# Kernel optimization log

Hardware: AMD Instinct MI355X
Metric: run time of the kernel (lower is better)

## Reference

```python
import jax, jax.numpy as jnp
import numpy as np

N = 50000          # nodes
E = 800000         # edges (avg degree 16)
NFEAT = 128        # dim_touched / gcn_nfeat
NHID = 96
NCLASS = 64
EXTRA = 32         # extra MLP-only features
NHID1, NHID2 = 128, 64
NN = 70            # top-k threshold rank
EPS = 1e-5         # BatchNorm1d eps


def setup_inputs() -> dict:
    key = jax.random.key(0)
    ks = jax.random.split(key, 24)
    x = jax.random.normal(ks[0], (N, NFEAT + EXTRA + 1), jnp.float32)
    grp = jax.random.randint(ks[1], (N,), 0, 2).astype(jnp.float32)
    x = x.at[:, -1].set(grp)  # last column is the group flag (target_group == 0)
    row = jax.random.randint(ks[2], (E,), 0, N, dtype=jnp.int32)
    col = jax.random.randint(ks[3], (E,), 0, N, dtype=jnp.int32)
    val = jax.random.uniform(ks[4], (E,), jnp.float32)

    def p(k, shape):
        return (jax.random.normal(k, shape, jnp.float32) * 0.05)

    return dict(
        x=x, row=row, col=col, val=val,
        W1=p(ks[5], (NFEAT, NHID)), b1=p(ks[6], (NHID,)),
        W2=p(ks[7], (NHID, NHID)), b2=p(ks[8], (NHID,)),
        W3=p(ks[9], (NHID, NHID)), b3=p(ks[10], (NHID,)),
        W4=p(ks[11], (NHID, NHID)), b4=p(ks[12], (NHID,)),
        W5=p(ks[13], (NHID, NCLASS)), b5=p(ks[14], (NCLASS,)),
        M1w=p(ks[15], (NCLASS + EXTRA, NHID1)), M1b=p(ks[16], (NHID1,)),
        M2w=p(ks[17], (NHID1, NHID2)), M2b=p(ks[18], (NHID2,)),
        M3w=p(ks[19], (NHID2, 1)), M3b=p(ks[20], (1,)),
    )


def _bn(h):
    # fresh BatchNorm1d in training mode, affine at default init (gamma=1, beta=0)
    m = jnp.mean(h, axis=0)
    v = jnp.mean((h - m) ** 2, axis=0)  # biased variance, as used for normalization
    return (h - m) * jax.lax.rsqrt(v + EPS)


def _gc(h, row, col, val, W, b):
    # GraphConvolution: spmm(adj, h @ W) + b, adj in COO form
    s = h @ W                                            # [N, out]
    msg = val[:, None] * s[col]                          # [E, out]
    agg = jax.ops.segment_sum(msg, row, num_segments=N)  # [N, out]
    return agg + b


def reference(x, row, col, val, W1, b1, W2, b2, W3, b3, W4, b4, W5, b5,
              M1w, M1b, M2w, M2b, M3w, M3b):
    h = x[:, :NFEAT]
    h = _bn(jax.nn.relu(_gc(h, row, col, val, W1, b1)))
    h = _bn(jax.nn.relu(_gc(h, row, col, val, W2, b2)))
    h = _bn(jax.nn.relu(_gc(h, row, col, val, W3, b3)))
    h = _bn(jax.nn.relu(_gc(h, row, col, val, W4, b4)))
    h = jax.nn.relu(_gc(h, row, col, val, W5, b5))        # [N, NCLASS]

    feat = jnp.concatenate([h, x[:, NFEAT:-1]], axis=1)   # [N, NCLASS+EXTRA]
    m = jax.nn.relu(feat @ M1w + M1b)
    m = jax.nn.relu(m @ M2w + M2b)
    m = m @ M3w + M3b                                     # [N, 1]

    # mask out target_group rows with the global min
    m = jnp.where(x[:, -1:] == 0.0, jnp.min(m), m)        # [N, 1]

    # top-70 threshold: value at descending rank NN
    thresh = jax.lax.top_k(m[:, 0], NN + 1)[0][NN]
    recip = jax.lax.stop_gradient(1.0 / m)                # torch reciprocal on detach()
    mask = jnp.where(m > thresh, recip, jnp.zeros_like(m))
    return m * mask
```

## Files before the change

kernel.cpp:

```cpp
#include <hip/hip_runtime.h>
#include <cstdint>
#include <cstddef>

#define XLD 161
#define GA  3072

typedef float f4u __attribute__((ext_vector_type(4), aligned(4)));
typedef float f4a __attribute__((ext_vector_type(4)));
typedef float f3u __attribute__((ext_vector_type(3), aligned(4)));
typedef float f2a __attribute__((ext_vector_type(2)));

__global__ void hist_kernel(const int* __restrict__ row, int* __restrict__ cnt, int E) {
    for (int e = blockIdx.x * blockDim.x + threadIdx.x; e < E; e += gridDim.x * blockDim.x)
        atomicAdd(&cnt[row[e]], 1);
}

__global__ __launch_bounds__(256)
void scan1_kernel(const int* __restrict__ cnt, int* __restrict__ offs,
                  int* __restrict__ bsums, int n) {
    int t = threadIdx.x;
    int gid = blockIdx.x * 256 + t;
    int v = (gid < n) ? cnt[gid] : 0;
    int x = v;
#pragma unroll
    for (int o = 1; o < 64; o <<= 1) { int y = __shfl_up(x, o); if ((t & 63) >= o) x += y; }
    __shared__ int ws[4];
    if ((t & 63) == 63) ws[t >> 6] = x;
    __syncthreads();
    int add = 0;
    for (int w = 0; w < (t >> 6); w++) add += ws[w];
    int incl = x + add;
    if (gid < n) offs[gid] = incl - v;
    if (t == 255) bsums[blockIdx.x] = incl;
}

__global__ __launch_bounds__(256)
void scan2_kernel(int* __restrict__ bsums, int nb) {
    int t = threadIdx.x;
    int v = (t < nb) ? bsums[t] : 0;
    int x = v;
#pragma unroll
    for (int o = 1; o < 64; o <<= 1) { int y = __shfl_up(x, o); if ((t & 63) >= o) x += y; }
    __shared__ int ws[4];
    if ((t & 63) == 63) ws[t >> 6] = x;
    __syncthreads();
    int add = 0;
    for (int w = 0; w < (t >> 6); w++) add += ws[w];
    if (t < nb) bsums[t] = x + add - v;
}

__global__ void scan3_kernel(int* __restrict__ offs, int* __restrict__ cursor,
                             const int* __restrict__ bsums, int n, int E) {
    int gid = blockIdx.x * 256 + threadIdx.x;
    if (gid < n) {
        int o = offs[gid] + bsums[blockIdx.x];
        offs[gid] = o;
        cursor[gid] = o;
    }
    if (gid == 0) offs[n] = E;
}

__global__ void scatter_kernel(const int* __restrict__ row, const int* __restrict__ col,
                               const float* __restrict__ val, int* __restrict__ cursor,
                               int2* __restrict__ cvA, int E) {
    for (int e = blockIdx.x * blockDim.x + threadIdx.x; e < E; e += gridDim.x * blockDim.x) {
        int r = row[e];
        int p = atomicAdd(&cursor[r], 1);
        cvA[p] = make_int2(col[e], __float_as_int(val[e]));
    }
}

template <int LC, bool WVS>
__global__ __launch_bounds__(256)
void aggP(const float* __restrict__ S, int ldS, const int* __restrict__ offs,
          const int2* __restrict__ cvA,
          float* __restrict__ Aout, float* __restrict__ vout, int n) {
    int lane = threadIdx.x & 63;
    int lg   = lane & 31;
    int grp  = threadIdx.x >> 5;
    int sh   = lane & 32;

    for (int node = blockIdx.x * 8 + grp; node < n; node += gridDim.x * 8) {
        int e0 = offs[node], e1 = offs[node + 1];
        float acc[LC];
#pragma unroll
        for (int a = 0; a < LC; a++) acc[a] = 0.f;
        float vsum = 0.f;

        for (int e = e0; e < e1; e += 32) {
            int   idx = e + lg;
            int2  cv = (idx < e1) ? cvA[idx] : make_int2(0, 0);
            int   ce = cv.x;
            float ve = __int_as_float(cv.y);
            int   cnt = min(32, e1 - e);
#pragma unroll 8
            for (int j = 0; j < cnt; j++) {
                int   c = __shfl(ce, sh + j);
                float v = __shfl(ve, sh + j);
                const float* srow = S + (size_t)c * ldS + LC * lg;
                if (LC == 3) {
                    f3u g = *(const f3u*)srow;
                    acc[0] = fmaf(v, g[0], acc[0]);
                    acc[1] = fmaf(v, g[1], acc[1]);
                    acc[2] = fmaf(v, g[2], acc[2]);
                } else {
                    f4u g = *(const f4u*)srow;
                    acc[0] = fmaf(v, g[0], acc[0]);
                    acc[1] = fmaf(v, g[1], acc[1]);
                    acc[2] = fmaf(v, g[2], acc[2]);
                    acc[3] = fmaf(v, g[3], acc[3]);
                }
                vsum += v;
            }
        }

        float* orow = Aout + (size_t)node * (32 * LC) + LC * lg;
        if (LC == 3) {
            f3u o; o[0] = acc[0]; o[1] = acc[1]; o[2] = acc[2];
            *(f3u*)orow = o;
        } else {
            f4u o; o[0] = acc[0]; o[1] = acc[1]; o[2] = acc[2]; o[3] = acc[3];
            *(f4u*)orow = o;
        }
        if (WVS && lg == 0) vout[node] = vsum;
    }
}

__global__ __launch_bounds__(256)
void aggB(const float* __restrict__ S, const int* __restrict__ offs,
          const int2* __restrict__ cvA, const float* __restrict__ bias,
          float* __restrict__ Hout, float* __restrict__ vout,
          float* __restrict__ pbuf, int n) {
    __shared__ float sS[96], sQ[96];
    int t = threadIdx.x;
    if (t < 96) { sS[t] = 0.f; sQ[t] = 0.f; }
    __syncthreads();
    int lane = t & 63, lg = lane & 31, grp = t >> 5, sh = lane & 32;
    float bb[3];
    bb[0] = bias[3 * lg]; bb[1] = bias[3 * lg + 1]; bb[2] = bias[3 * lg + 2];
    float ps[3] = {0.f, 0.f, 0.f}, pq[3] = {0.f, 0.f, 0.f};

    for (int node = blockIdx.x * 8 + grp; node < n; node += gridDim.x * 8) {
        int e0 = offs[node], e1 = offs[node + 1];
        float acc[3] = {0.f, 0.f, 0.f};
        float vsum = 0.f;
        for (int e = e0; e < e1; e += 32) {
            int   idx = e + lg;
            int2  cv = (idx < e1) ? cvA[idx] : make_int2(0, 0);
            int   ce = cv.x;
            float ve = __int_as_float(cv.y);
            int   cnt = min(32, e1 - e);
#pragma unroll 8
            for (int j = 0; j < cnt; j++) {
                int   c = __shfl(ce, sh + j);
                float v = __shfl(ve, sh + j);
                const float* srow = S + (size_t)c * 96 + 3 * lg;
                f3u g = *(const f3u*)srow;
                acc[0] = fmaf(v, g[0], acc[0]);
                acc[1] = fmaf(v, g[1], acc[1]);
                acc[2] = fmaf(v, g[2], acc[2]);
                vsum += v;
            }
        }
        float* orow = Hout + (size_t)node * 96 + 3 * lg;
        f3u o;
#pragma unroll
        for (int a = 0; a < 3; a++) {
            float v = fmaxf(acc[a] + bb[a], 0.f);
            o[a] = v;
            ps[a] += v; pq[a] += v * v;
        }
        *(f3u*)orow = o;
        if (lg == 0) vout[node] = vsum;
    }
#pragma unroll
    for (int a = 0; a < 3; a++) {
        atomicAdd(&sS[3 * lg + a], ps[a]);
        atomicAdd(&sQ[3 * lg + a], pq[a]);
    }
    __syncthreads();
    if (t < 96) {
        pbuf[(size_t)t * GA + blockIdx.x]        = sS[t];
        pbuf[(size_t)(96 + t) * GA + blockIdx.x] = sQ[t];
    }
}

__global__ __launch_bounds__(256)
void bn_reduce(const float* __restrict__ pbuf, float* __restrict__ bsum,
               float* __restrict__ bsumsq) {
    int j = blockIdx.x;
    const float* rowp = pbuf + (size_t)j * GA;
    float s = 0.f;
    for (int i = threadIdx.x; i < GA; i += 256) s += rowp[i];
#pragma unroll
    for (int o = 32; o; o >>= 1) s += __shfl_down(s, o);
    __shared__ float ws[4];
    if ((threadIdx.x & 63) == 0) ws[threadIdx.x >> 6] = s;
    __syncthreads();
    if (threadIdx.x == 0) {
        float tot = ws[0] + ws[1] + ws[2] + ws[3];
        if (j < 96) bsum[j] = tot; else bsumsq[j - 96] = tot;
    }
}

__global__ __launch_bounds__(256)
void aggC(const float* __restrict__ S, const int* __restrict__ offs,
          const int2* __restrict__ cvA, const float* __restrict__ bias,
          const float* __restrict__ cb, const float* __restrict__ vsum,
          float* __restrict__ Hout, int n) {
    int lane = threadIdx.x & 63, lg = lane & 31, grp = threadIdx.x >> 5, sh = lane & 32;
    float bb0 = bias[2 * lg], bb1 = bias[2 * lg + 1];
    float cc0 = cb[2 * lg],   cc1 = cb[2 * lg + 1];

    for (int node = blockIdx.x * 8 + grp; node < n; node += gridDim.x * 8) {
        int e0 = offs[node], e1 = offs[node + 1];
        float a0 = 0.f, a1 = 0.f;
        for (int e = e0; e < e1; e += 32) {
            int   idx = e + lg;
            int2  cv = (idx < e1) ? cvA[idx] : make_int2(0, 0);
            int   ce = cv.x;
            float ve = __int_as_float(cv.y);
            int   cnt = min(32, e1 - e);
#pragma unroll 8
            for (int j = 0; j < cnt; j++) {
                int   c = __shfl(ce, sh + j);
                float v = __shfl(ve, sh + j);
                f2a g = *(const f2a*)(S + (size_t)c * 64 + 2 * lg);
                a0 = fmaf(v, g[0], a0);
                a1 = fmaf(v, g[1], a1);
            }
        }
        float vs = vsum[node];
        f2a o;
        o[0] = fmaxf(a0 + vs * cc0 + bb0, 0.f);
        o[1] = fmaxf(a1 + vs * cc1 + bb1, 0.f);
        *(f2a*)(Hout + (size_t)node * 64 + 2 * lg) = o;
    }
}

template <int CT>
__device__ inline void ldw(const float* p, float* wv) {
    if constexpr (CT == 4) { *(f4a*)wv = *(const f4a*)p; }
    else if constexpr (CT == 6) { *(f3u*)wv = *(const f3u*)p; *(f3u*)(wv + 3) = *(const f3u*)(p + 3); }
    else { *(f4a*)wv = *(const f4a*)p; *(f4a*)(wv + 4) = *(const f4a*)(p + 4); }
}

template <int K, int C, bool DOBN, bool HASCB, bool LIN = false, bool DOT = false>
__global__ __launch_bounds__(256)
void gemmF(const float* __restrict__ A1, int ld1, int split,
           const float* __restrict__ A2, int ld2,
           const float* __restrict__ W, const float* __restrict__ bias,
           const float* __restrict__ cbv, const float* __restrict__ vsum,
           float* __restrict__ Out, float* __restrict__ bsum,
           float* __restrict__ bsumsq, int n) {
    constexpr int CT = C / 16;
    __shared__ float Wc[16 * C];
    __shared__ float At[16][68];
    __shared__ float redS[DOBN ? C : 1];
    __shared__ float redQ[DOBN ? C : 1];

    int t  = threadIdx.x;
    int tc = t & 15, tr = t >> 4;
    int row0 = blockIdx.x * 64;

    if (DOBN && t < C) { redS[t] = 0.f; redQ[t] = 0.f; }

    int srow = t >> 2;
    int gr = row0 + srow; if (gr >= n) gr = n - 1;
    int kh = (t & 3) * 4;

    float acc[4][CT];
#pragma unroll
    for (int i = 0; i < 4; i++)
#pragma unroll
        for (int c = 0; c < CT; c++) acc[i][c] = 0.f;

    for (int kb = 0; kb < K; kb += 16) {
        __syncthreads();
        for (int i = t * 4; i < 16 * C; i += 1024)
            *(f4a*)&Wc[i] = *(const f4u*)&W[(size_t)kb * C + i];
        {
            int kg = kb + kh;
            const float* src = (kg < split) ? (A1 + (size_t)gr * ld1 + kg)
                                            : (A2 + (size_t)gr * ld2 + (kg - split));
            f4u v = *(const f4u*)src;
#pragma unroll
            for (int e = 0; e < 4; e++) At[kh + e][srow] = v[e];
        }
        __syncthreads();
#pragma unroll
        for (int kk = 0; kk < 16; kk++) {
            f4a av = *(const f4a*)&At[kk][tr * 4];
            float wv[CT];
            ldw<CT>(&Wc[kk * C + tc * CT], wv);
#pragma unroll
            for (int i = 0; i < 4; i++)
#pragma unroll
                for (int c = 0; c < CT; c++) acc[i][c] = fmaf(av[i], wv[c], acc[i][c]);
        }
    }

    if constexpr (DOT) {
        float bb2[CT], ww[CT];
#pragma unroll
        for (int c = 0; c < CT; c++) { bb2[c] = bias[tc * CT + c]; ww[c] = cbv[tc * CT + c]; }
        float b3 = vsum[0];
        float lmin = 3.4e38f;
#pragma unroll
        for (int i = 0; i < 4; i++) {
            float d = 0.f;
#pragma unroll
            for (int c = 0; c < CT; c++) d = fmaf(fmaxf(acc[i][c] + bb2[c], 0.f), ww[c], d);
            d += __shfl_xor(d, 1); d += __shfl_xor(d, 2);
            d += __shfl_xor(d, 4); d += __shfl_xor(d, 8);
            int r = row0 + tr * 4 + i;
            if (tc == 0 && r < n) {
                float mv = d + b3;
                Out[r] = mv;
                lmin = fminf(lmin, mv);
            }
        }
        __shared__ float smin[16];
        if (tc == 0) smin[tr] = lmin;
        __syncthreads();
        if (t == 0) {
            float mn = smin[0];
#pragma unroll
            for (int i2 = 1; i2 < 16; i2++) mn = fminf(mn, smin[i2]);
            unsigned u = __float_as_uint(mn);
            unsigned key = (u >> 31) ? ~u : (u | 0x80000000u);
            atomicMin((unsigned*)bsum, key);
        }
        return;
    }

    float bb[CT], cc[CT];
#pragma unroll
    for (int c = 0; c < CT; c++) {
        bb[c] = LIN ? 0.f : bias[tc * CT + c];
        cc[c] = HASCB ? cbv[tc * CT + c] : 0.f;
    }
    float ps[CT], pq[CT];
#pragma unroll
    for (int c = 0; c < CT; c++) { ps[c] = 0.f; pq[c] = 0.f; }

#pragma unroll
    for (int i = 0; i < 4; i++) {
        int r = row0 + tr * 4 + i;
        if (r < n) {
            float vs = HASCB ? vsum[r] : 0.f;
            float* o = Out + (size_t)r * C + tc * CT;
#pragma unroll
            for (int c = 0; c < CT; c++) {
                float v = acc[i][c] + vs * cc[c] + bb[c];
                if (!LIN) v = fmaxf(v, 0.f);
                o[c] = v;
                if (DOBN) { ps[c] += v; pq[c] += v * v; }
            }
        }
    }
    if (DOBN) {
#pragma unroll
        for (int c = 0; c < CT; c++) {
            ps[c] += __shfl_xor(ps[c], 16);
            ps[c] += __shfl_xor(ps[c], 32);
            pq[c] += __shfl_xor(pq[c], 16);
            pq[c] += __shfl_xor(pq[c], 32);
        }
        if ((t & 48) == 0) {
#pragma unroll
            for (int c = 0; c < CT; c++) {
                atomicAdd(&redS[tc * CT + c], ps[c]);
                atomicAdd(&redQ[tc * CT + c], pq[c]);
            }
        }
        __syncthreads();
        if (t < C) {
            atomicAdd(&bsum[t], redS[t]);
            atomicAdd(&bsumsq[t], redQ[t]);
        }
    }
}

template <int C>
__global__ __launch_bounds__(256)
void fold_kernel(const float* __restrict__ W, float* __restrict__ bsum,
                 float* __restrict__ bsumsq, float* __restrict__ Wf,
                 float* __restrict__ cb, int N) {
    __shared__ float mean[96], inv[96];
    int t = threadIdx.x;
    float rn = 1.0f / (float)N;
    if (t < 96) {
        float mu  = bsum[t] * rn;
        float var = bsumsq[t] * rn - mu * mu;
        mean[t] = mu;
        inv[t]  = rsqrtf(var + 1e-5f);
        bsum[t] = 0.f;
        bsumsq[t] = 0.f;
    }
    __syncthreads();
    for (int i = t; i < 96 * C; i += 256) {
        int k = i / C;
        Wf[i] = inv[k] * W[i];
    }
    if (t < C) {
        float s = 0.f;
        for (int k = 0; k < 96; k++) s += mean[k] * inv[k] * W[k * C + t];
        cb[t] = -s;
    }
}

__global__ void where_kernel(const float* __restrict__ x, float* __restrict__ m,
                             const unsigned* __restrict__ gmin, int n) {
    int i = blockIdx.x * blockDim.x + threadIdx.x;
    if (i < n) {
        unsigned k = *gmin;
        unsigned u = (k >> 31) ? (k ^ 0x80000000u) : ~k;
        float g = __uint_as_float(u);
        if (x[(size_t)i * XLD + 160] == 0.0f) m[i] = g;
    }
}

__device__ inline unsigned fkey(float f) {
    unsigned u = __float_as_uint(f);
    return (u >> 31) ? ~u : (u | 0x80000000u);
}

__global__ __launch_bounds__(256)
void sel_hist8(const float* __restrict__ m, unsigned* __restrict__ h0, int n) {
    __shared__ unsigned lh[256];
    int t = threadIdx.x;
    lh[t] = 0u;
    __syncthreads();
    for (int i = blockIdx.x * 256 + t; i < n; i += gridDim.x * 256)
        atomicAdd(&lh[fkey(m[i]) >> 24], 1u);
    __syncthreads();
    if (lh[t]) atomicAdd(&h0[t], lh[t]);
}

__global__ __launch_bounds__(256)
void sel_pick8(const unsigned* __restrict__ h, const unsigned* __restrict__ kres,
               int kconst, unsigned* __restrict__ outb, unsigned* __restrict__ outk) {
    int t = threadIdx.x;
    int bin = 255 - t;
    unsigned k = kres ? *kres : (unsigned)kconst;
    unsigned c = h[bin];
    unsigned x = c;
#pragma unroll
    for (int o = 1; o < 64; o <<= 1) { unsigned y = __shfl_up(x, o); if ((t & 63) >= o) x += y; }
    __shared__ unsigned ws[4];
    if ((t & 63) == 63) ws[t >> 6] = x;
    __syncthreads();
    unsigned add = 0;
    for (int w = 0; w < (t >> 6); w++) add += ws[w];
    unsigned incl = x + add, excl = incl - c;
    if (excl < k && k <= incl) { *outb = (unsigned)bin; *outk = k - excl; }
}

__global__ __launch_bounds__(256)
void sel_hist8b(const float* __restrict__ m, const unsigned* __restrict__ pick,
                unsigned* __restrict__ h1, int n) {
    __shared__ unsigned lh[256];
    int t = threadIdx.x;
    lh[t] = 0u;
    __syncthreads();
    unsigned b0 = pick[0];
    for (int i = blockIdx.x * 256 + t; i < n; i += gridDim.x * 256) {
        unsigned key = fkey(m[i]);
        if ((key >> 24) == b0) atomicAdd(&lh[(key >> 16) & 255u], 1u);
    }
    __syncthreads();
    if (lh[t]) atomicAdd(&h1[t], lh[t]);
}

__global__ void sel_collect(const float* __restrict__ m, const unsigned* __restrict__ pick,
                            unsigned* __restrict__ sbuf, unsigned* __restrict__ scnt, int n) {
    unsigned pfx = (pick[0] << 8) | pick[2];
    for (int i = blockIdx.x * blockDim.x + threadIdx.x; i < n; i += gridDim.x * blockDim.x) {
        unsigned key = fkey(m[i]);
        if ((key >> 16) == pfx) sbuf[atomicAdd(scnt, 1u)] = key;
    }
}

__global__ __launch_bounds__(1024)
void sel_final(const unsigned* __restrict__ sbuf, const unsigned* __restrict__ scnt,
               const unsigned* __restrict__ pick, float* __restrict__ thresh) {
    __shared__ unsigned hist[256];
    __shared__ unsigned spfx;
    __shared__ int skk;
    int t = threadIdx.x;
    int ns = (int)*scnt;
    if (t == 0) { spfx = ((pick[0] << 8) | pick[2]) << 16; skk = (int)pick[3]; }
    __syncthreads();
    for (int pass = 0; pass < 2; ++pass) {
        if (t < 256) hist[t] = 0u;
        __syncthreads();
        int shift = 8 - 8 * pass;
        unsigned pfxmask = (pass == 0) ? 0xFFFF0000u : 0xFFFFFF00u;
        unsigned pfx = spfx;
        for (int i = t; i < ns; i += 1024) {
            unsigned key = sbuf[i];
            if ((key & pfxmask) == pfx) atomicAdd(&hist[(key >> shift) & 255u], 1u);
        }
        __syncthreads();
        if (t == 0) {
            int cum = 0, kk = skk, chosen = 0;
            for (int b = 255; b >= 0; b--) {
                cum += (int)hist[b];
                if (cum >= kk) { chosen = b; kk -= (cum - (int)hist[b]); break; }
            }
            spfx = pfx | ((unsigned)chosen << shift);
            skk = kk;
        }
        __syncthreads();
    }
    if (t == 0) {
        unsigned key = spfx;
        unsigned u = (key >> 31) ? (key ^ 0x80000000u) : ~key;
        *thresh = __uint_as_float(u);
    }
}

__global__ void mask_kernel(const float* __restrict__ m, const float* __restrict__ thresh,
                            float* __restrict__ out, int n) {
    int i = blockIdx.x * blockDim.x + threadIdx.x;
    if (i < n) {
        float t = *thresh, v = m[i];
        out[i] = (v > t) ? v * (1.0f / v) : 0.0f;
    }
}

extern "C" void kernel_launch(void* const* d_in, const int* in_sizes, int n_in,
                              void* d_out, int out_size, void* d_ws, size_t ws_size,
                              hipStream_t stream) {
    const float* x   = (const float*)d_in[0];
    const int*   row = (const int*)d_in[1];
    const int*   col = (const int*)d_in[2];
    const float* val = (const float*)d_in[3];
    const float* W1  = (const float*)d_in[4];
    const float* b1  = (const float*)d_in[5];
    const float* W2  = (const float*)d_in[6];
    const float* b2  = (const float*)d_in[7];
    const float* W3  = (const float*)d_in[8];
    const float* b3  = (const float*)d_in[9];
    const float* W4  = (const float*)d_in[10];
    const float* b4  = (const float*)d_in[11];
    const float* W5  = (const float*)d_in[12];
    const float* b5  = (const float*)d_in[13];
    const float* M1w = (const float*)d_in[14];
    const float* M1b = (const float*)d_in[15];
    const float* M2w = (const float*)d_in[16];
    const float* M2b = (const float*)d_in[17];
    const float* M3w = (const float*)d_in[18];
    const float* M3b = (const float*)d_in[19];

    const int n = in_sizes[0] / XLD;
    const int E = in_sizes[1];

    char* ws = (char*)d_ws;
    size_t off = 0;
    auto carve = [&](size_t bytes) -> void* {
        void* p = ws + off;
        off = (off + bytes + 255) & ~(size_t)255;
        return p;
    };
    int*      offs   = (int*)carve((size_t)(n + 1) * 4);
    int*      cursor = (int*)carve((size_t)n * 4);
    int*      bsums  = (int*)carve(256 * 4);
    int2*     cvA    = (int2*)carve((size_t)E * 8);
    float*    h      = (float*)carve((size_t)n * 96 * 4);
    float*    big    = (float*)carve((size_t)n * 128 * 4);
    float*    Wf     = (float*)carve(96 * 96 * 4);
    float*    stats  = (float*)carve(192 * 4);
    float*    cb     = (float*)carve(96 * 4);
    float*    vsum   = (float*)carve((size_t)n * 4);
    float*    m      = (float*)carve((size_t)n * 4);
    unsigned* gmin   = (unsigned*)carve(4);
    float*    thresh = (float*)carve(4);
    unsigned* h0     = (unsigned*)carve(256 * 4);
    unsigned* h1     = (unsigned*)carve(256 * 4);
    unsigned* sbuf   = (unsigned*)carve((size_t)n * 4);
    unsigned* scnt   = (unsigned*)carve(4);
    unsigned* pick   = (unsigned*)carve(16);
    float*    pbuf   = (float*)carve((size_t)192 * GA * 4);
    float* bsum   = stats;
    float* bsumsq = stats + 96;

    hipMemsetAsync(cursor, 0, (size_t)n * 4, stream);
    hipMemsetAsync(stats, 0, 192 * 4, stream);
    hipMemsetAsync(gmin, 0xFF, 4, stream);
    hipMemsetAsync(h0, 0, 256 * 4, stream);
    hipMemsetAsync(h1, 0, 256 * 4, stream);
    hipMemsetAsync(scnt, 0, 4, stream);

    const int nb = (n + 255) / 256;
    hist_kernel<<<512, 256, 0, stream>>>(row, cursor, E);
    scan1_kernel<<<nb, 256, 0, stream>>>(cursor, offs, bsums, n);
    scan2_kernel<<<1, 256, 0, stream>>>(bsums, nb);
    scan3_kernel<<<nb, 256, 0, stream>>>(offs, cursor, bsums, n, E);
    scatter_kernel<<<512, 256, 0, stream>>>(row, col, val, cursor, cvA, E);

    const int gB = (n + 63) / 64;

    gemmF<128, 96, false, false, true><<<gB, 256, 0, stream>>>(x, XLD, 128, x, XLD,
        W1, b1, nullptr, nullptr, big, bsum, bsumsq, n);
    aggB<<<GA, 256, 0, stream>>>(big, offs, cvA, b1, h, vsum, pbuf, n);
    bn_reduce<<<192, 256, 0, stream>>>(pbuf, bsum, bsumsq);

    fold_kernel<96><<<1, 256, 0, stream>>>(W2, bsum, bsumsq, Wf, cb, n);
    aggP<3, false><<<GA, 256, 0, stream>>>(h, 96, offs, cvA, big, nullptr, n);
    gemmF<96, 96, true, true><<<gB, 256, 0, stream>>>(big, 96, 96, big, 96,
        Wf, b2, cb, vsum, h, bsum, bsumsq, n);

    fold_kernel<96><<<1, 256, 0, stream>>>(W3, bsum, bsumsq, Wf, cb, n);
    aggP<3, false><<<GA, 256, 0, stream>>>(h, 96, offs, cvA, big, nullptr, n);
    gemmF<96, 96, true, true><<<gB, 256, 0, stream>>>(big, 96, 96, big, 96,
        Wf, b3, cb, vsum, h, bsum, bsumsq, n);

    fold_kernel<96><<<1, 256, 0, stream>>>(W4, bsum, bsumsq, Wf, cb, n);
    aggP<3, false><<<GA, 256, 0, stream>>>(h, 96, offs, cvA, big, nullptr, n);
    gemmF<96, 96, true, true><<<gB, 256, 0, stream>>>(big, 96, 96, big, 96,
        Wf, b4, cb, vsum, h, bsum, bsumsq, n);

    fold_kernel<64><<<1, 256, 0, stream>>>(W5, bsum, bsumsq, Wf, cb, n);
    gemmF<96, 64, false, false, true><<<gB, 256, 0, stream>>>(h, 96, 96, h, 96,
        Wf, b5, nullptr, nullptr, big, bsum, bsumsq, n);
    aggC<<<GA, 256, 0, stream>>>(big, offs, cvA, b5, cb, vsum, h, n);

    gemmF<96, 128, false, false><<<gB, 256, 0, stream>>>(h, 64, 64, x + 128, XLD,
        M1w, M1b, nullptr, nullptr, big, bsum, bsumsq, n);
    gemmF<128, 64, false, false, false, true><<<gB, 256, 0, stream>>>(big, 128, 128, big, 128,
        M2w, M2b, M3w, M3b, m, (float*)gmin, nullptr, n);

    where_kernel<<<(n + 255) / 256, 256, 0, stream>>>(x, m, gmin, n);

    sel_hist8<<<64, 256, 0, stream>>>(m, h0, n);
    sel_pick8<<<1, 256, 0, stream>>>(h0, nullptr, 71, &pick[0], &pick[1]);
    sel_hist8b<<<64, 256, 0, stream>>>(m, pick, h1, n);
    sel_pick8<<<1, 256, 0, stream>>>(h1, &pick[1], 0, &pick[2], &pick[3]);
    sel_collect<<<64, 256, 0, stream>>>(m, pick, sbuf, scnt, n);
    sel_final<<<1, 1024, 0, stream>>>(sbuf, scnt, pick, thresh);

    mask_kernel<<<(n + 255) / 256, 256, 0, stream>>>(m, thresh, (float*)d_out, n);
}
```

Baseline: 737.0 us.

## Fuse MLP layers into one kernel, merge where with histogram, restructure BN partials

Fuses the two MLP GEMMs (M1 and M2 plus the M3 dot) into a single kernel that keeps the 64x128 hidden tile in shared memory, so the N x 128 intermediate never goes to global memory. Merges the where-masking pass into the first selection histogram kernel, removing one launch and one pass over m. Transposes the BN partial-sum buffer to a block-major layout, reduces it with 64 blocks using atomics, and cuts the aggregation grid from 3072 to 2048 blocks. The fused kernel uses more shared memory per block, which may lower occupancy.

```diff
diff --git a/kernel.cpp b/kernel.cpp
--- a/kernel.cpp
+++ b/kernel.cpp
@@ -3,7 +3,7 @@
 #include <cstddef>
 
 #define XLD 161
-#define GA  3072
+#define GA  2048
 
 typedef float f4u __attribute__((ext_vector_type(4), aligned(4)));
 typedef float f4a __attribute__((ext_vector_type(4)));
@@ -180,26 +180,19 @@
     }
     __syncthreads();
     if (t < 96) {
-        pbuf[(size_t)t * GA + blockIdx.x]        = sS[t];
-        pbuf[(size_t)(96 + t) * GA + blockIdx.x] = sQ[t];
-    }
-}
-
-__global__ __launch_bounds__(256)
-void bn_reduce(const float* __restrict__ pbuf, float* __restrict__ bsum,
-               float* __restrict__ bsumsq) {
-    int j = blockIdx.x;
-    const float* rowp = pbuf + (size_t)j * GA;
+        pbuf[(size_t)blockIdx.x * 192 + t]      = sS[t];
+        pbuf[(size_t)blockIdx.x * 192 + 96 + t] = sQ[t];
+    }
+}
+
+__global__ __launch_bounds__(256)
+void bn_reduce(const float* __restrict__ pbuf, float* __restrict__ stats) {
+    int t = threadIdx.x;
     float s = 0.f;
-    for (int i = threadIdx.x; i < GA; i += 256) s += rowp[i];
-#pragma unroll
-    for (int o = 32; o; o >>= 1) s += __shfl_down(s, o);
-    __shared__ float ws[4];
-    if ((threadIdx.x & 63) == 0) ws[threadIdx.x >> 6] = s;
-    __syncthreads();
-    if (threadIdx.x == 0) {
-        float tot = ws[0] + ws[1] + ws[2] + ws[3];
-        if (j < 96) bsum[j] = tot; else bsumsq[j - 96] = tot;
+    if (t < 192) {
+        for (int pb = blockIdx.x; pb < GA; pb += gridDim.x)
+            s += pbuf[(size_t)pb * 192 + t];
+        atomicAdd(&stats[t], s);
     }
 }
 
@@ -245,7 +238,7 @@
     else { *(f4a*)wv = *(const f4a*)p; *(f4a*)(wv + 4) = *(const f4a*)(p + 4); }
 }
 
-template <int K, int C, bool DOBN, bool HASCB, bool LIN = false, bool DOT = false>
+template <int K, int C, bool DOBN, bool HASCB, bool LIN = false>
 __global__ __launch_bounds__(256)
 void gemmF(const float* __restrict__ A1, int ld1, int split,
            const float* __restrict__ A2, int ld2,
@@ -300,40 +293,6 @@
         }
     }
 
-    if constexpr (DOT) {
-        float bb2[CT], ww[CT];
-#pragma unroll
-        for (int c = 0; c < CT; c++) { bb2[c] = bias[tc * CT + c]; ww[c] = cbv[tc * CT + c]; }
-        float b3 = vsum[0];
-        float lmin = 3.4e38f;
-#pragma unroll
-        for (int i = 0; i < 4; i++) {
-            float d = 0.f;
-#pragma unroll
-            for (int c = 0; c < CT; c++) d = fmaf(fmaxf(acc[i][c] + bb2[c], 0.f), ww[c], d);
-            d += __shfl_xor(d, 1); d += __shfl_xor(d, 2);
-            d += __shfl_xor(d, 4); d += __shfl_xor(d, 8);
-            int r = row0 + tr * 4 + i;
-            if (tc == 0 && r < n) {
-                float mv = d + b3;
-                Out[r] = mv;
-                lmin = fminf(lmin, mv);
-            }
-        }
-        __shared__ float smin[16];
-        if (tc == 0) smin[tr] = lmin;
-        __syncthreads();
-        if (t == 0) {
-            float mn = smin[0];
-#pragma unroll
-            for (int i2 = 1; i2 < 16; i2++) mn = fminf(mn, smin[i2]);
-            unsigned u = __float_as_uint(mn);
-            unsigned key = (u >> 31) ? ~u : (u | 0x80000000u);
-            atomicMin((unsigned*)bsum, key);
-        }
-        return;
-    }
-
     float bb[CT], cc[CT];
 #pragma unroll
     for (int c = 0; c < CT; c++) {
@@ -379,6 +338,129 @@
             atomicAdd(&bsum[t], redS[t]);
             atomicAdd(&bsumsq[t], redQ[t]);
         }
+    }
+}
+
+__global__ __launch_bounds__(256)
+void gemmM12(const float* __restrict__ h, const float* __restrict__ xe,
+             const float* __restrict__ M1w, const float* __restrict__ M1b,
+             const float* __restrict__ M2w, const float* __restrict__ M2b,
+             const float* __restrict__ M3w, const float* __restrict__ M3b,
+             float* __restrict__ m, unsigned* __restrict__ gmin, int n) {
+    __shared__ float Wc[16 * 128];
+    __shared__ float At[16][68];
+    __shared__ float T[64][132];
+
+    int t = threadIdx.x;
+    int tc = t & 15, tr = t >> 4;
+    int row0 = blockIdx.x * 64;
+    int srow = t >> 2;
+    int gr = row0 + srow; if (gr >= n) gr = n - 1;
+    int kh = (t & 3) * 4;
+
+    float acc1[4][8];
+#pragma unroll
+    for (int i = 0; i < 4; i++)
+#pragma unroll
+        for (int c = 0; c < 8; c++) acc1[i][c] = 0.f;
+
+    for (int kb = 0; kb < 96; kb += 16) {
+        __syncthreads();
+        for (int i = t * 4; i < 16 * 128; i += 1024)
+            *(f4a*)&Wc[i] = *(const f4u*)&M1w[(size_t)kb * 128 + i];
+        {
+            int kg = kb + kh;
+            const float* src = (kg < 64) ? (h + (size_t)gr * 64 + kg)
+                                         : (xe + (size_t)gr * XLD + (kg - 64));
+            f4u v = *(const f4u*)src;
+#pragma unroll
+            for (int e = 0; e < 4; e++) At[kh + e][srow] = v[e];
+        }
+        __syncthreads();
+#pragma unroll
+        for (int kk = 0; kk < 16; kk++) {
+            f4a av = *(const f4a*)&At[kk][tr * 4];
+            float wv[8];
+            *(f4a*)wv = *(const f4a*)&Wc[kk * 128 + tc * 8];
+            *(f4a*)(wv + 4) = *(const f4a*)&Wc[kk * 128 + tc * 8 + 4];
+#pragma unroll
+            for (int i = 0; i < 4; i++)
+#pragma unroll
+                for (int c = 0; c < 8; c++) acc1[i][c] = fmaf(av[i], wv[c], acc1[i][c]);
+        }
+    }
+    float b1v[8];
+#pragma unroll
+    for (int c = 0; c < 8; c++) b1v[c] = M1b[tc * 8 + c];
+#pragma unroll
+    for (int i = 0; i < 4; i++) {
+        f4a w0, w1;
+#pragma unroll
+        for (int c = 0; c < 4; c++) {
+            w0[c] = fmaxf(acc1[i][c] + b1v[c], 0.f);
+            w1[c] = fmaxf(acc1[i][c + 4] + b1v[c + 4], 0.f);
+        }
+        *(f4a*)&T[tr * 4 + i][tc * 8]     = w0;
+        *(f4a*)&T[tr * 4 + i][tc * 8 + 4] = w1;
+    }
+
+    float acc2[4][4];
+#pragma unroll
+    for (int i = 0; i < 4; i++)
+#pragma unroll
+        for (int c = 0; c < 4; c++) acc2[i][c] = 0.f;
+
+    for (int kb = 0; kb < 128; kb += 16) {
+        __syncthreads();
+        *(f4a*)&Wc[t * 4] = *(const f4u*)&M2w[(size_t)kb * 64 + t * 4];
+        __syncthreads();
+#pragma unroll
+        for (int k4 = 0; k4 < 16; k4 += 4) {
+            f4a av4[4];
+#pragma unroll
+            for (int i = 0; i < 4; i++)
+                av4[i] = *(const f4a*)&T[tr * 4 + i][kb + k4];
+#pragma unroll
+            for (int q = 0; q < 4; q++) {
+                f4a wv = *(const f4a*)&Wc[(k4 + q) * 64 + tc * 4];
+#pragma unroll
+                for (int i = 0; i < 4; i++)
+#pragma unroll
+                    for (int c = 0; c < 4; c++)
+                        acc2[i][c] = fmaf(av4[i][q], wv[c], acc2[i][c]);
+            }
+        }
+    }
+
+    float bb2[4], ww[4];
+#pragma unroll
+    for (int c = 0; c < 4; c++) { bb2[c] = M2b[tc * 4 + c]; ww[c] = M3w[tc * 4 + c]; }
+    float b3 = M3b[0];
+    float lmin = 3.4e38f;
+#pragma unroll
+    for (int i = 0; i < 4; i++) {
+        float d = 0.f;
+#pragma unroll
+        for (int c = 0; c < 4; c++) d = fmaf(fmaxf(acc2[i][c] + bb2[c], 0.f), ww[c], d);
+        d += __shfl_xor(d, 1); d += __shfl_xor(d, 2);
+        d += __shfl_xor(d, 4); d += __shfl_xor(d, 8);
+        int r = row0 + tr * 4 + i;
+        if (tc == 0 && r < n) {
+            float mv = d + b3;
+            m[r] = mv;
+            lmin = fminf(lmin, mv);
+        }
+    }
+    __shared__ float smin[16];
+    if (tc == 0) smin[tr] = lmin;
+    __syncthreads();
+    if (t == 0) {
+        float mn = smin[0];
+#pragma unroll
+        for (int i2 = 1; i2 < 16; i2++) mn = fminf(mn, smin[i2]);
+        unsigned u = __float_as_uint(mn);
+        unsigned key = (u >> 31) ? ~u : (u | 0x80000000u);
+        atomicMin(gmin, key);
     }
 }
 
@@ -410,30 +492,26 @@
     }
 }
 
-__global__ void where_kernel(const float* __restrict__ x, float* __restrict__ m,
-                             const unsigned* __restrict__ gmin, int n) {
-    int i = blockIdx.x * blockDim.x + threadIdx.x;
-    if (i < n) {
-        unsigned k = *gmin;
-        unsigned u = (k >> 31) ? (k ^ 0x80000000u) : ~k;
-        float g = __uint_as_float(u);
-        if (x[(size_t)i * XLD + 160] == 0.0f) m[i] = g;
-    }
-}
-
 __device__ inline unsigned fkey(float f) {
     unsigned u = __float_as_uint(f);
     return (u >> 31) ? ~u : (u | 0x80000000u);
 }
 
 __global__ __launch_bounds__(256)
-void sel_hist8(const float* __restrict__ m, unsigned* __restrict__ h0, int n) {
+void where_hist(const float* __restrict__ x, float* __restrict__ m,
+                const unsigned* __restrict__ gmin, unsigned* __restrict__ h0, int n) {
     __shared__ unsigned lh[256];
     int t = threadIdx.x;
     lh[t] = 0u;
     __syncthreads();
-    for (int i = blockIdx.x * 256 + t; i < n; i += gridDim.x * 256)
-        atomicAdd(&lh[fkey(m[i]) >> 24], 1u);
+    unsigned k = *gmin;
+    unsigned u = (k >> 31) ? (k ^ 0x80000000u) : ~k;
+    float g = __uint_as_float(u);
+    for (int i = blockIdx.x * 256 + t; i < n; i += gridDim.x * 256) {
+        float mv = m[i];
+        if (x[(size_t)i * XLD + 160] == 0.0f) { mv = g; m[i] = mv; }
+        atomicAdd(&lh[fkey(mv) >> 24], 1u);
+    }
     __syncthreads();
     if (lh[t]) atomicAdd(&h0[t], lh[t]);
 }
@@ -582,7 +660,7 @@
     unsigned* sbuf   = (unsigned*)carve((size_t)n * 4);
     unsigned* scnt   = (unsigned*)carve(4);
     unsigned* pick   = (unsigned*)carve(16);
-    float*    pbuf   = (float*)carve((size_t)192 * GA * 4);
+    float*    pbuf   = (float*)carve((size_t)GA * 192 * 4);
     float* bsum   = stats;
     float* bsumsq = stats + 96;
 
@@ -605,7 +683,7 @@
     gemmF<128, 96, false, false, true><<<gB, 256, 0, stream>>>(x, XLD, 128, x, XLD,
         W1, b1, nullptr, nullptr, big, bsum, bsumsq, n);
     aggB<<<GA, 256, 0, stream>>>(big, offs, cvA, b1, h, vsum, pbuf, n);
-    bn_reduce<<<192, 256, 0, stream>>>(pbuf, bsum, bsumsq);
+    bn_reduce<<<64, 256, 0, stream>>>(pbuf, stats);
 
     fold_kernel<96><<<1, 256, 0, stream>>>(W2, bsum, bsumsq, Wf, cb, n);
     aggP<3, false><<<GA, 256, 0, stream>>>(h, 96, offs, cvA, big, nullptr, n);
@@ -627,14 +705,10 @@
         Wf, b5, nullptr, nullptr, big, bsum, bsumsq, n);
     aggC<<<GA, 256, 0, stream>>>(big, offs, cvA, b5, cb, vsum, h, n);
 
-    gemmF<96, 128, false, false><<<gB, 256, 0, stream>>>(h, 64, 64, x + 128, XLD,
-        M1w, M1b, nullptr, nullptr, big, bsum, bsumsq, n);
-    gemmF<128, 64, false, false, false, true><<<gB, 256, 0, stream>>>(big, 128, 128, big, 128,
-        M2w, M2b, M3w, M3b, m, (float*)gmin, nullptr, n);
-
-    where_kernel<<<(n + 255) / 256, 256, 0, stream>>>(x, m, gmin, n);
-
-    sel_hist8<<<64, 256, 0, stream>>>(m, h0, n);
+    gemmM12<<<gB, 256, 0, stream>>>(h, x + 128, M1w, M1b, M2w, M2b, M3w, M3b, m, gmin, n);
+
+    where_hist<<<64, 256, 0, stream>>>(x, m, gmin, h0, n);
+
     sel_pick8<<<1, 256, 0, stream>>>(h0, nullptr, 71, &pick[0], &pick[1]);
     sel_hist8b<<<64, 256, 0, stream>>>(m, pick, h1, n);
     sel_pick8<<<1, 256, 0, stream>>>(h1, &pick[1], 0, &pick[2], &pick[3]);
```

After: 736.8 us. Within noise of the previous version (-0.0%).

## Transpose BN partial buffer, fuse where-mask into histogram, widen CSR build grids

Applied to the files above, without the earlier changes.

The per-block BatchNorm partial sums are now stored block-major. A 64-block reduction accumulates all 192 columns with coalesced reads and atomically adds into the stats buffer, replacing 192 single-row reduction blocks. The group-mask where step is folded into the first selection histogram kernel, which removes one launch and one pass over m. The histogram and scatter kernels for CSR construction also get four times as many blocks. Atomic accumulation into stats depends on the earlier memset to zero, and float summation order changes.

```diff
diff --git a/kernel.cpp b/kernel.cpp
--- a/kernel.cpp
+++ b/kernel.cpp
@@ -180,26 +180,19 @@
     }
     __syncthreads();
     if (t < 96) {
-        pbuf[(size_t)t * GA + blockIdx.x]        = sS[t];
-        pbuf[(size_t)(96 + t) * GA + blockIdx.x] = sQ[t];
-    }
-}
-
-__global__ __launch_bounds__(256)
-void bn_reduce(const float* __restrict__ pbuf, float* __restrict__ bsum,
-               float* __restrict__ bsumsq) {
-    int j = blockIdx.x;
-    const float* rowp = pbuf + (size_t)j * GA;
+        pbuf[(size_t)blockIdx.x * 192 + t]      = sS[t];
+        pbuf[(size_t)blockIdx.x * 192 + 96 + t] = sQ[t];
+    }
+}
+
+__global__ __launch_bounds__(256)
+void bn_reduce(const float* __restrict__ pbuf, float* __restrict__ stats) {
+    int t = threadIdx.x;
     float s = 0.f;
-    for (int i = threadIdx.x; i < GA; i += 256) s += rowp[i];
-#pragma unroll
-    for (int o = 32; o; o >>= 1) s += __shfl_down(s, o);
-    __shared__ float ws[4];
-    if ((threadIdx.x & 63) == 0) ws[threadIdx.x >> 6] = s;
-    __syncthreads();
-    if (threadIdx.x == 0) {
-        float tot = ws[0] + ws[1] + ws[2] + ws[3];
-        if (j < 96) bsum[j] = tot; else bsumsq[j - 96] = tot;
+    if (t < 192) {
+        for (int pb = blockIdx.x; pb < GA; pb += gridDim.x)
+            s += pbuf[(size_t)pb * 192 + t];
+        atomicAdd(&stats[t], s);
     }
 }
 
@@ -410,30 +403,26 @@
     }
 }
 
-__global__ void where_kernel(const float* __restrict__ x, float* __restrict__ m,
-                             const unsigned* __restrict__ gmin, int n) {
-    int i = blockIdx.x * blockDim.x + threadIdx.x;
-    if (i < n) {
-        unsigned k = *gmin;
-        unsigned u = (k >> 31) ? (k ^ 0x80000000u) : ~k;
-        float g = __uint_as_float(u);
-        if (x[(size_t)i * XLD + 160] == 0.0f) m[i] = g;
-    }
-}
-
 __device__ inline unsigned fkey(float f) {
     unsigned u = __float_as_uint(f);
     return (u >> 31) ? ~u : (u | 0x80000000u);
 }
 
 __global__ __launch_bounds__(256)
-void sel_hist8(const float* __restrict__ m, unsigned* __restrict__ h0, int n) {
+void where_hist(const float* __restrict__ x, float* __restrict__ m,
+                const unsigned* __restrict__ gmin, unsigned* __restrict__ h0, int n) {
     __shared__ unsigned lh[256];
     int t = threadIdx.x;
     lh[t] = 0u;
     __syncthreads();
-    for (int i = blockIdx.x * 256 + t; i < n; i += gridDim.x * 256)
-        atomicAdd(&lh[fkey(m[i]) >> 24], 1u);
+    unsigned k = *gmin;
+    unsigned u = (k >> 31) ? (k ^ 0x80000000u) : ~k;
+    float g = __uint_as_float(u);
+    for (int i = blockIdx.x * 256 + t; i < n; i += gridDim.x * 256) {
+        float mv = m[i];
+        if (x[(size_t)i * XLD + 160] == 0.0f) { mv = g; m[i] = mv; }
+        atomicAdd(&lh[fkey(mv) >> 24], 1u);
+    }
     __syncthreads();
     if (lh[t]) atomicAdd(&h0[t], lh[t]);
 }
@@ -582,7 +571,7 @@
     unsigned* sbuf   = (unsigned*)carve((size_t)n * 4);
     unsigned* scnt   = (unsigned*)carve(4);
     unsigned* pick   = (unsigned*)carve(16);
-    float*    pbuf   = (float*)carve((size_t)192 * GA * 4);
+    float*    pbuf   = (float*)carve((size_t)GA * 192 * 4);
     float* bsum   = stats;
     float* bsumsq = stats + 96;
 
@@ -594,18 +583,18 @@
     hipMemsetAsync(scnt, 0, 4, stream);
 
     const int nb = (n + 255) / 256;
-    hist_kernel<<<512, 256, 0, stream>>>(row, cursor, E);
+    hist_kernel<<<2048, 256, 0, stream>>>(row, cursor, E);
     scan1_kernel<<<nb, 256, 0, stream>>>(cursor, offs, bsums, n);
     scan2_kernel<<<1, 256, 0, stream>>>(bsums, nb);
     scan3_kernel<<<nb, 256, 0, stream>>>(offs, cursor, bsums, n, E);
-    scatter_kernel<<<512, 256, 0, stream>>>(row, col, val, cursor, cvA, E);
+    scatter_kernel<<<2048, 256, 0, stream>>>(row, col, val, cursor, cvA, E);
 
     const int gB = (n + 63) / 64;
 
     gemmF<128, 96, false, false, true><<<gB, 256, 0, stream>>>(x, XLD, 128, x, XLD,
         W1, b1, nullptr, nullptr, big, bsum, bsumsq, n);
     aggB<<<GA, 256, 0, stream>>>(big, offs, cvA, b1, h, vsum, pbuf, n);
-    bn_reduce<<<192, 256, 0, stream>>>(pbuf, bsum, bsumsq);
+    bn_reduce<<<64, 256, 0, stream>>>(pbuf, stats);
 
     fold_kernel<96><<<1, 256, 0, stream>>>(W2, bsum, bsumsq, Wf, cb, n);
     aggP<3, false><<<GA, 256, 0, stream>>>(h, 96, offs, cvA, big, nullptr, n);
@@ -632,9 +621,8 @@
     gemmF<128, 64, false, false, false, true><<<gB, 256, 0, stream>>>(big, 128, 128, big, 128,
         M2w, M2b, M3w, M3b, m, (float*)gmin, nullptr, n);
 
-    where_kernel<<<(n + 255) / 256, 256, 0, stream>>>(x, m, gmin, n);
-
-    sel_hist8<<<64, 256, 0, stream>>>(m, h0, n);
+    where_hist<<<64, 256, 0, stream>>>(x, m, gmin, h0, n);
+
     sel_pick8<<<1, 256, 0, stream>>>(h0, nullptr, 71, &pick[0], &pick[1]);
     sel_hist8b<<<64, 256, 0, stream>>>(m, pick, h1, n);
     sel_pick8<<<1, 256, 0, stream>>>(h1, &pick[1], 0, &pick[2], &pick[3]);
```

After: 744.5 us. About the same (+1.0%).
